# Performance work log

Hardware: AMD Instinct MI355X
Metric: run time of the kernel (lower is better)

The kernel has to match this reference:

```python
import jax, jax.numpy as jnp
import numpy as np

B, H, W, C = 4, 64, 64, 64
C8 = C // 8

def setup_inputs() -> dict:
    key = jax.random.key(0)
    ks = jax.random.split(key, 7)
    x = jax.random.normal(ks[0], (B, H, W, C), dtype=jnp.float32)
    # 1x1 conv weights (channels_first), Glorot-ish scale
    Wf = jax.random.normal(ks[1], (C, C8), dtype=jnp.float32) * (1.0 / np.sqrt(C))
    bf = jnp.zeros((C8,), dtype=jnp.float32)
    Wg = jax.random.normal(ks[2], (C, C8), dtype=jnp.float32) * (1.0 / np.sqrt(C))
    bg = jnp.zeros((C8,), dtype=jnp.float32)
    Wh = jax.random.normal(ks[3], (C, C), dtype=jnp.float32) * (1.0 / np.sqrt(C))
    bh = jnp.zeros((C,), dtype=jnp.float32)
    # original inits gamma=0.0 (output == input); use 0.5 so attention path is exercised
    gamma = jnp.float32(0.5)
    return {"x": x, "Wf": Wf, "bf": bf, "Wg": Wg, "bg": bg, "Wh": Wh, "bh": bh, "gamma": gamma}

def reference(x, Wf, bf, Wg, bg, Wh, bh, gamma):
    Bq, Hq, Wq, Cq = x.shape
    N = Hq * Wq
    # Permute((3,2,1)): (B,H,W,C) -> (B,C,W,H)
    xp = jnp.transpose(x, (0, 3, 2, 1))
    xf = xp.reshape(Bq, Cq, N)  # (B, C, N)
    # 1x1 convs (channels_first) == per-pixel channel matmuls, relu activation
    f = jax.nn.relu(jnp.einsum('ck,bcn->bkn', Wf, xf) + bf[None, :, None])  # (B, C/8, N)
    g = jax.nn.relu(jnp.einsum('ck,bcn->bkn', Wg, xf) + bg[None, :, None])  # (B, C/8, N)
    h = jax.nn.relu(jnp.einsum('cd,bcn->bdn', Wh, xf) + bh[None, :, None])  # (B, C, N)
    # s = g^T f : (B, N, N)
    s = jnp.einsum('bcn,bcm->bnm', g, f)
    b_att = jax.nn.softmax(s, axis=-1)
    # o = h @ b_att : (B, C, N)
    o = jnp.einsum('bck,bkn->bcn', h, b_att)
    y = gamma * o.reshape(xp.shape) + xp
    # Permute((3,2,1)) back: (B,C,W,H) -> (B,H,W,C)
    return jnp.transpose(y, (0, 3, 2, 1))
```

## Files before the change

kernel.cpp:

```cpp
#include <hip/hip_runtime.h>
#include <math.h>

#define B_  4
#define HH  64
#define WW  64
#define CC  64
#define C8_ 8
#define NN  4096
#define BN  (B_*NN)
#define NS  4
#define LOG2E 1.44269504088896340736f

typedef _Float16 half8 __attribute__((ext_vector_type(8)));
typedef float f32x4 __attribute__((ext_vector_type(4)));

#define SWZ(row, kbyte) (((((row) << 7) + (kbyte))) ^ (((row) & 7) << 4))

__global__ __launch_bounds__(256) void prep_kernel(
    const float* __restrict__ x,  const float* __restrict__ Wf, const float* __restrict__ bf,
    const float* __restrict__ Wg, const float* __restrict__ bg, const float* __restrict__ Wh,
    const float* __restrict__ bh, float* __restrict__ f_out, float* __restrict__ g2_out,
    float* __restrict__ h_out)
{
    __shared__ float sWh[CC*CC];
    __shared__ float sWf[CC*C8_];
    __shared__ float sWg[CC*C8_];
    __shared__ float sbf[C8_], sbg[C8_], sbh[CC];
    const int t = threadIdx.x;

    for (int i = t; i < CC*CC/4; i += 256) ((float4*)sWh)[i] = ((const float4*)Wh)[i];
    for (int i = t; i < CC*C8_/4; i += 256) {
        ((float4*)sWf)[i] = ((const float4*)Wf)[i];
        ((float4*)sWg)[i] = ((const float4*)Wg)[i];
    }
    if (t < C8_) { sbf[t] = bf[t]; sbg[t] = bg[t]; }
    if (t < CC)  sbh[t] = bh[t];
    __syncthreads();

    const int p = blockIdx.x * 256 + t;
    const int b = p >> 12;
    const int n = p & (NN - 1);
    const int h = n & 63, w = n >> 6;
    const float4* xr4 = (const float4*)(x + (((size_t)(b*HH + h)*WW + w) * CC));

    float fa[C8_], ga[C8_], ha[CC];
    #pragma unroll
    for (int j = 0; j < C8_; ++j) { fa[j] = sbf[j]; ga[j] = sbg[j]; }
    #pragma unroll
    for (int d = 0; d < CC; ++d) ha[d] = sbh[d];

    #pragma unroll
    for (int c4 = 0; c4 < CC/4; ++c4) {
        float4 v = xr4[c4];
        float xs[4] = {v.x, v.y, v.z, v.w};
        #pragma unroll
        for (int u = 0; u < 4; ++u) {
            const int c = c4*4 + u;
            const float xc = xs[u];
            #pragma unroll
            for (int j = 0; j < C8_; ++j) {
                fa[j] = fmaf(sWf[c*C8_ + j], xc, fa[j]);
                ga[j] = fmaf(sWg[c*C8_ + j], xc, ga[j]);
            }
            #pragma unroll
            for (int d = 0; d < CC; ++d)
                ha[d] = fmaf(sWh[c*CC + d], xc, ha[d]);
        }
    }

    float* fp = f_out  + (size_t)p * C8_;
    float* gp = g2_out + (size_t)p * C8_;
    #pragma unroll
    for (int j4 = 0; j4 < 2; ++j4) {
        float4 fo, go;
        fo.x = fmaxf(fa[j4*4+0], 0.f); fo.y = fmaxf(fa[j4*4+1], 0.f);
        fo.z = fmaxf(fa[j4*4+2], 0.f); fo.w = fmaxf(fa[j4*4+3], 0.f);
        go.x = fmaxf(ga[j4*4+0], 0.f) * LOG2E; go.y = fmaxf(ga[j4*4+1], 0.f) * LOG2E;
        go.z = fmaxf(ga[j4*4+2], 0.f) * LOG2E; go.w = fmaxf(ga[j4*4+3], 0.f) * LOG2E;
        ((float4*)fp)[j4] = fo;
        ((float4*)gp)[j4] = go;
    }
    #pragma unroll
    for (int d = 0; d < CC; ++d)
        h_out[((size_t)(b*CC + d))*NN + n] = fmaxf(ha[d], 0.f);
}

__global__ __launch_bounds__(512) void pass1_kernel(
    const float* __restrict__ f_in, const float* __restrict__ g2_in,
    float* __restrict__ pm_out, float* __restrict__ pz_out)
{
    __shared__ float sF[128*C8_];
    __shared__ float pm[8][64], pz[8][64];
    const int t  = threadIdx.x;
    const int bi = blockIdx.x;
    const int ktile = bi & 63;
    const int b  = (bi >> 6) & 3;
    const int ns = bi >> 8;
    const int k0 = ktile << 6;
    const int kk = t & 63;
    const int q  = t >> 6;
    const int k  = k0 + kk;

    const float4* gp = (const float4*)(g2_in + ((size_t)b*NN + k)*C8_);
    const float4 g0 = gp[0], g1 = gp[1];
    const float4* fb = ((const float4*)f_in) + (size_t)b*8192 + ns*2048;

    float m = 0.f, z = 0.f;
    for (int T = 0; T < 8; ++T) {
        __syncthreads();
        if (t < 256) ((float4*)sF)[t] = fb[T*256 + t];
        __syncthreads();
        const float4* sF4 = (const float4*)sF;
        #pragma unroll 4
        for (int i = 0; i < 16; ++i) {
            const int nl = q*16 + i;
            const float4 f0 = sF4[nl*2], f1 = sF4[nl*2 + 1];
            float s = g0.x*f0.x + g0.y*f0.y + g0.z*f0.z + g0.w*f0.w
                    + g1.x*f1.x + g1.y*f1.y + g1.z*f1.z + g1.w*f1.w;
            if (s > m) { z = z * exp2f(m - s) + 1.f; m = s; }
            else       { z += exp2f(s - m); }
        }
    }
    pm[q][kk] = m; pz[q][kk] = z;
    __syncthreads();
    if (t < 64) {
        float M = pm[0][t];
        #pragma unroll
        for (int qq = 1; qq < 8; ++qq) M = fmaxf(M, pm[qq][t]);
        float Z = 0.f;
        #pragma unroll
        for (int qq = 0; qq < 8; ++qq) Z += pz[qq][t] * exp2f(pm[qq][t] - M);
        pm_out[(size_t)ns*BN + b*NN + k0 + t] = M;
        pz_out[(size_t)ns*BN + b*NN + k0 + t] = Z;
    }
}

__global__ __launch_bounds__(256) void lse_combine_kernel(
    const float* __restrict__ pm, const float* __restrict__ pz,
    float* __restrict__ L2_out)
{
    const int r = blockIdx.x * 256 + threadIdx.x;
    float M = pm[r];
    #pragma unroll
    for (int ns = 1; ns < NS; ++ns) M = fmaxf(M, pm[(size_t)ns*BN + r]);
    float Z = 0.f;
    #pragma unroll
    for (int ns = 0; ns < NS; ++ns)
        Z += pz[(size_t)ns*BN + r] * exp2f(pm[(size_t)ns*BN + r] - M);
    L2_out[r] = M + log2f(Z);
}

#define OFF_SWH 0
#define OFF_SWL 16384
#define OFF_SHH 32768
#define OFF_SHL 40960
#define OFF_SG  49152
#define OFF_SL  51200
#define LDS_SZ  51456

__global__ __launch_bounds__(256, 3) void pass2_kernel(
    const float* __restrict__ f_in, const float* __restrict__ g2_in,
    const float* __restrict__ h_in, const float* __restrict__ L2_in,
    float* __restrict__ opart, int ksplit)
{
    __shared__ __align__(16) unsigned char lds[LDS_SZ];

    const int t     = threadIdx.x;
    const int bi    = blockIdx.x;
    const int nt    = bi & 31;
    const int b     = (bi >> 5) & 3;
    const int chunk = bi >> 7;
    const int n0    = nt << 7;
    const int kchunk = NN / ksplit;
    const int kbase0 = chunk * kchunk;
    const int ktiles = kchunk >> 6;

    const int lane = t & 63, wid = t >> 6;
    const int wn = wid & 1, kh = wid >> 1;
    const int nw = t & 127, kh2 = t >> 7;
    const int sc = t >> 2,  skq = t & 3;

    const float4* fp4 = (const float4*)(f_in + ((size_t)b*NN + n0 + nw)*C8_);
    const float4 fA = fp4[0], fB = fp4[1];

    f32x4 acc[4][4] = {};

    for (int kt = 0; kt < ktiles; ++kt) {
        const int kb = kbase0 + (kt << 6);
        __syncthreads();
        if (t < 128) ((float4*)(lds + OFF_SG))[t] =
            ((const float4*)(g2_in + ((size_t)b*NN + kb)*C8_))[t];
        if (t < 16) ((float4*)(lds + OFF_SL))[t] =
            ((const float4*)(L2_in + (size_t)b*NN + kb))[t];
        {
            const float* hr = h_in + ((size_t)(b*CC + sc))*NN + kb + skq*16;
            float hv[16];
            #pragma unroll
            for (int j = 0; j < 4; ++j) {
                float4 v = ((const float4*)hr)[j];
                hv[j*4+0] = v.x; hv[j*4+1] = v.y; hv[j*4+2] = v.z; hv[j*4+3] = v.w;
            }
            #pragma unroll
            for (int half = 0; half < 2; ++half) {
                union { _Float16 h[8]; uint4 u; } ph, pl;
                #pragma unroll
                for (int j = 0; j < 8; ++j) {
                    float v = hv[half*8 + j];
                    _Float16 hi = (_Float16)v;
                    ph.h[j] = hi;
                    pl.h[j] = (_Float16)(v - (float)hi);
                }
                const int kbyte = (skq*16 + half*8) * 2;
                *(uint4*)(lds + OFF_SHH + SWZ(sc, kbyte)) = ph.u;
                *(uint4*)(lds + OFF_SHL + SWZ(sc, kbyte)) = pl.u;
            }
        }
        __syncthreads();
        {
            const float4* sG4 = (const float4*)(lds + OFF_SG);
            const float*  sLf = (const float*)(lds + OFF_SL);
            #pragma unroll
            for (int kk8 = 0; kk8 < 4; ++kk8) {
                union { _Float16 h[8]; uint4 u; } wh, wl;
                #pragma unroll
                for (int j = 0; j < 8; ++j) {
                    const int kkk = kh2*32 + kk8*8 + j;
                    const float4 q0 = sG4[kkk*2], q1 = sG4[kkk*2+1];
                    float s = q0.x*fA.x + q0.y*fA.y + q0.z*fA.z + q0.w*fA.w
                            + q1.x*fB.x + q1.y*fB.y + q1.z*fB.z + q1.w*fB.w;
                    float wv = exp2f(s - sLf[kkk]);
                    _Float16 hi = (_Float16)wv;
                    wh.h[j] = hi;
                    wl.h[j] = (_Float16)(wv - (float)hi);
                }
                const int kbyte = (kh2*32 + kk8*8) * 2;
                *(uint4*)(lds + OFF_SWH + SWZ(nw, kbyte)) = wh.u;
                *(uint4*)(lds + OFF_SWL + SWZ(nw, kbyte)) = wl.u;
            }
        }
        __syncthreads();
        {
            const int kbyteg = (kh*32 + ((lane >> 4) << 3)) << 1;
            half8 Ah[4], Al[4];
            #pragma unroll
            for (int ai = 0; ai < 4; ++ai) {
                const int n = wn*64 + ai*16 + (lane & 15);
                Ah[ai] = *(const half8*)(lds + OFF_SWH + SWZ(n, kbyteg));
                Al[ai] = *(const half8*)(lds + OFF_SWL + SWZ(n, kbyteg));
            }
            #pragma unroll
            for (int bj = 0; bj < 4; ++bj) {
                const int c = bj*16 + (lane & 15);
                const half8 Bh = *(const half8*)(lds + OFF_SHH + SWZ(c, kbyteg));
                const half8 Bl = *(const half8*)(lds + OFF_SHL + SWZ(c, kbyteg));
                #pragma unroll
                for (int ai = 0; ai < 4; ++ai) {
                    acc[ai][bj] = __builtin_amdgcn_mfma_f32_16x16x32_f16(Ah[ai], Bh, acc[ai][bj], 0, 0, 0);
                    acc[ai][bj] = __builtin_amdgcn_mfma_f32_16x16x32_f16(Ah[ai], Bl, acc[ai][bj], 0, 0, 0);
                    acc[ai][bj] = __builtin_amdgcn_mfma_f32_16x16x32_f16(Al[ai], Bh, acc[ai][bj], 0, 0, 0);
                }
            }
        }
    }

    __syncthreads();
    float* scratch = (float*)lds;
    if (kh == 1) {
        #pragma unroll
        for (int ai = 0; ai < 4; ++ai)
            #pragma unroll
            for (int bj = 0; bj < 4; ++bj)
                #pragma unroll
                for (int r = 0; r < 4; ++r) {
                    const int nloc = ai*16 + (lane >> 4)*4 + r;
                    const int c    = bj*16 + (lane & 15);
                    scratch[wn*4096 + nloc*64 + c] = acc[ai][bj][r];
                }
    }
    __syncthreads();
    if (kh == 0) {
        float* op = opart + (((size_t)chunk*B_ + b)*NN + n0 + wn*64)*CC;
        #pragma unroll
        for (int ai = 0; ai < 4; ++ai)
            #pragma unroll
            for (int bj = 0; bj < 4; ++bj)
                #pragma unroll
                for (int r = 0; r < 4; ++r) {
                    const int nloc = ai*16 + (lane >> 4)*4 + r;
                    const int c    = bj*16 + (lane & 15);
                    op[(size_t)nloc*CC + c] = acc[ai][bj][r] + scratch[wn*4096 + nloc*64 + c];
                }
    }
}

__global__ __launch_bounds__(256) void epi_kernel(
    const float* __restrict__ x, const float* __restrict__ opart,
    const float* __restrict__ gamma_p, float* __restrict__ y, int nchunks)
{
    const int idx = blockIdx.x * 256 + threadIdx.x;
    const float gm = gamma_p[0];
    const int c4 = idx & 15;
    const int n  = (idx >> 4) & (NN - 1);
    const int b  = idx >> 16;
    float4 o; o.x = 0.f; o.y = 0.f; o.z = 0.f; o.w = 0.f;
    for (int ch = 0; ch < nchunks; ++ch) {
        const float4 v = ((const float4*)opart)[((size_t)(ch*B_ + b)*NN + n)*16 + c4];
        o.x += v.x; o.y += v.y; o.z += v.z; o.w += v.w;
    }
    const int h = n & 63, w = n >> 6;
    const size_t xi = ((size_t)((b*HH + h)*WW + w)*CC >> 2) + c4;
    const float4 xv = ((const float4*)x)[xi];
    float4 r;
    r.x = fmaf(gm, o.x, xv.x);
    r.y = fmaf(gm, o.y, xv.y);
    r.z = fmaf(gm, o.z, xv.z);
    r.w = fmaf(gm, o.w, xv.w);
    ((float4*)y)[xi] = r;
}

extern "C" void kernel_launch(void* const* d_in, const int* in_sizes, int n_in,
                              void* d_out, int out_size, void* d_ws, size_t ws_size,
                              hipStream_t stream)
{
    const float* x     = (const float*)d_in[0];
    const float* Wf    = (const float*)d_in[1];
    const float* bf    = (const float*)d_in[2];
    const float* Wg    = (const float*)d_in[3];
    const float* bg    = (const float*)d_in[4];
    const float* Wh    = (const float*)d_in[5];
    const float* bh    = (const float*)d_in[6];
    const float* gamma = (const float*)d_in[7];
    float* out = (float*)d_out;

    float* f_buf  = (float*)d_ws;
    float* g2_buf = f_buf  + (size_t)BN*C8_;
    float* h_buf  = g2_buf + (size_t)BN*C8_;
    float* L2_buf = h_buf  + (size_t)BN*CC;
    float* opart  = L2_buf + (size_t)BN;
    float* pm_buf = opart;
    float* pz_buf = opart + (size_t)NS*BN;

    const size_t fixed = (size_t)(BN*C8_*2 + BN*CC + BN);
    int ksplit = 1;
    if      (ws_size >= (fixed + (size_t)8*BN*CC) * 4) ksplit = 8;
    else if (ws_size >= (fixed + (size_t)4*BN*CC) * 4) ksplit = 4;
    else if (ws_size >= (fixed + (size_t)2*BN*CC) * 4) ksplit = 2;

    prep_kernel<<<BN/256, 256, 0, stream>>>(x, Wf, bf, Wg, bg, Wh, bh,
                                            f_buf, g2_buf, h_buf);
    pass1_kernel<<<NS*B_*64, 512, 0, stream>>>(f_buf, g2_buf, pm_buf, pz_buf);
    lse_combine_kernel<<<BN/256, 256, 0, stream>>>(pm_buf, pz_buf, L2_buf);
    pass2_kernel<<<128*ksplit, 256, 0, stream>>>(f_buf, g2_buf, h_buf, L2_buf,
                                                 opart, ksplit);
    epi_kernel<<<(BN*CC/4)/256, 256, 0, stream>>>(x, opart, gamma, out, ksplit);
}
```

Measured before the change: 207.4 us.

## Use MFMA for score computation, precomputed softmax bound, and restructured prep

The attention scores in pass2 now come from fp16 split-precision MFMA instructions instead of scalar dot products. This needs a per-tile staging of g and f in LDS, and the cross-warp k-split reduction is dropped. Pass1 uses a fixed upper bound (g dot per-batch channel max of f, found by atomicMax in prep) instead of an online running max, which removes branchy rescaling. The prep kernel is restructured to 32 pixels per block with channel groups spread across threads, which cuts register pressure. The maximum k-split drops from 8 to 4. The fixed-bound softmax risks underflow when scores fall far below the bound, and split fp16 scores may lose some accuracy.

New measurement: 180.3 us. 1.15x faster.

```diff
diff --git a/kernel.cpp b/kernel.cpp
--- a/kernel.cpp
+++ b/kernel.cpp
@@ -14,83 +14,121 @@
 typedef _Float16 half8 __attribute__((ext_vector_type(8)));
 typedef float f32x4 __attribute__((ext_vector_type(4)));
 
-#define SWZ(row, kbyte) (((((row) << 7) + (kbyte))) ^ (((row) & 7) << 4))
-
+#define SWZ(row, kbyte) ((((row) << 7) + (kbyte)) ^ (((row) & 7) << 4))
+
+__global__ void zero_fmax_kernel(unsigned* __restrict__ fmax_u) {
+    if (threadIdx.x < B_*C8_) fmax_u[threadIdx.x] = 0u;
+}
+
+#define XSTR 66
 __global__ __launch_bounds__(256) void prep_kernel(
     const float* __restrict__ x,  const float* __restrict__ Wf, const float* __restrict__ bf,
     const float* __restrict__ Wg, const float* __restrict__ bg, const float* __restrict__ Wh,
     const float* __restrict__ bh, float* __restrict__ f_out, float* __restrict__ g2_out,
-    float* __restrict__ h_out)
-{
+    float* __restrict__ h_out, unsigned* __restrict__ fmax_u)
+{
+    __shared__ float sX[32*XSTR];
     __shared__ float sWh[CC*CC];
     __shared__ float sWf[CC*C8_];
     __shared__ float sWg[CC*C8_];
-    __shared__ float sbf[C8_], sbg[C8_], sbh[CC];
-    const int t = threadIdx.x;
+    const int t  = threadIdx.x;
+    const int px = t & 31;
+    const int dg = t >> 5;
 
     for (int i = t; i < CC*CC/4; i += 256) ((float4*)sWh)[i] = ((const float4*)Wh)[i];
-    for (int i = t; i < CC*C8_/4; i += 256) {
-        ((float4*)sWf)[i] = ((const float4*)Wf)[i];
-        ((float4*)sWg)[i] = ((const float4*)Wg)[i];
-    }
-    if (t < C8_) { sbf[t] = bf[t]; sbg[t] = bg[t]; }
-    if (t < CC)  sbh[t] = bh[t];
+    if (t < 128) {
+        ((float4*)sWf)[t] = ((const float4*)Wf)[t];
+        ((float4*)sWg)[t] = ((const float4*)Wg)[t];
+    }
+
+    const int p0 = blockIdx.x * 32;
+    const int b  = p0 >> 12;
+    const int n0 = p0 & (NN - 1);
+    const int h0 = n0 & 63, w = n0 >> 6;
+
+    {
+        const int spx = t >> 3, cq = t & 7;
+        const float* xr = x + (((size_t)(b*HH + h0 + spx)*WW + w) * CC) + cq*8;
+        float4 v0 = ((const float4*)xr)[0], v1 = ((const float4*)xr)[1];
+        float* dst = sX + spx*XSTR + cq*8;
+        dst[0]=v0.x; dst[1]=v0.y; dst[2]=v0.z; dst[3]=v0.w;
+        dst[4]=v1.x; dst[5]=v1.y; dst[6]=v1.z; dst[7]=v1.w;
+    }
     __syncthreads();
 
-    const int p = blockIdx.x * 256 + t;
-    const int b = p >> 12;
-    const int n = p & (NN - 1);
-    const int h = n & 63, w = n >> 6;
-    const float4* xr4 = (const float4*)(x + (((size_t)(b*HH + h)*WW + w) * CC));
-
-    float fa[C8_], ga[C8_], ha[CC];
-    #pragma unroll
-    for (int j = 0; j < C8_; ++j) { fa[j] = sbf[j]; ga[j] = sbg[j]; }
-    #pragma unroll
-    for (int d = 0; d < CC; ++d) ha[d] = sbh[d];
-
-    #pragma unroll
-    for (int c4 = 0; c4 < CC/4; ++c4) {
-        float4 v = xr4[c4];
-        float xs[4] = {v.x, v.y, v.z, v.w};
+    const bool do_fg = dg < 2;
+    const float* sWfg = (dg == 0) ? sWf : sWg;
+    const float* bfg  = (dg == 0) ? bf  : bg;
+
+    float ha[8], fa[8];
+    #pragma unroll
+    for (int j = 0; j < 8; ++j) {
+        ha[j] = bh[dg*8 + j];
+        fa[j] = do_fg ? bfg[j] : 0.f;
+    }
+
+    const float* xrow = sX + px*XSTR;
+    #pragma unroll 4
+    for (int c = 0; c < CC; ++c) {
+        const float xc = xrow[c];
+        const float4 w0 = ((const float4*)sWh)[c*16 + dg*2];
+        const float4 w1 = ((const float4*)sWh)[c*16 + dg*2 + 1];
+        ha[0] = fmaf(w0.x, xc, ha[0]); ha[1] = fmaf(w0.y, xc, ha[1]);
+        ha[2] = fmaf(w0.z, xc, ha[2]); ha[3] = fmaf(w0.w, xc, ha[3]);
+        ha[4] = fmaf(w1.x, xc, ha[4]); ha[5] = fmaf(w1.y, xc, ha[5]);
+        ha[6] = fmaf(w1.z, xc, ha[6]); ha[7] = fmaf(w1.w, xc, ha[7]);
+        if (do_fg) {
+            const float4 f0 = ((const float4*)sWfg)[c*2];
+            const float4 f1 = ((const float4*)sWfg)[c*2 + 1];
+            fa[0] = fmaf(f0.x, xc, fa[0]); fa[1] = fmaf(f0.y, xc, fa[1]);
+            fa[2] = fmaf(f0.z, xc, fa[2]); fa[3] = fmaf(f0.w, xc, fa[3]);
+            fa[4] = fmaf(f1.x, xc, fa[4]); fa[5] = fmaf(f1.y, xc, fa[5]);
+            fa[6] = fmaf(f1.z, xc, fa[6]); fa[7] = fmaf(f1.w, xc, fa[7]);
+        }
+    }
+
+    const int p = p0 + px, n = n0 + px;
+    #pragma unroll
+    for (int j = 0; j < 8; ++j)
+        h_out[((size_t)(b*CC + dg*8 + j))*NN + n] = fmaxf(ha[j], 0.f);
+
+    float fo[8];
+    #pragma unroll
+    for (int j = 0; j < 8; ++j) fo[j] = fmaxf(fa[j], 0.f);
+    if (dg == 0) {
+        float4 a, c4;
+        a.x=fo[0]; a.y=fo[1]; a.z=fo[2]; a.w=fo[3];
+        c4.x=fo[4]; c4.y=fo[5]; c4.z=fo[6]; c4.w=fo[7];
+        ((float4*)(f_out + (size_t)p*C8_))[0] = a;
+        ((float4*)(f_out + (size_t)p*C8_))[1] = c4;
+    } else if (dg == 1) {
+        float4 a, c4;
+        a.x=fo[0]*LOG2E; a.y=fo[1]*LOG2E; a.z=fo[2]*LOG2E; a.w=fo[3]*LOG2E;
+        c4.x=fo[4]*LOG2E; c4.y=fo[5]*LOG2E; c4.z=fo[6]*LOG2E; c4.w=fo[7]*LOG2E;
+        ((float4*)(g2_out + (size_t)p*C8_))[0] = a;
+        ((float4*)(g2_out + (size_t)p*C8_))[1] = c4;
+    }
+
+    __syncthreads();
+    if (dg == 0) {
         #pragma unroll
-        for (int u = 0; u < 4; ++u) {
-            const int c = c4*4 + u;
-            const float xc = xs[u];
-            #pragma unroll
-            for (int j = 0; j < C8_; ++j) {
-                fa[j] = fmaf(sWf[c*C8_ + j], xc, fa[j]);
-                ga[j] = fmaf(sWg[c*C8_ + j], xc, ga[j]);
-            }
-            #pragma unroll
-            for (int d = 0; d < CC; ++d)
-                ha[d] = fmaf(sWh[c*CC + d], xc, ha[d]);
-        }
-    }
-
-    float* fp = f_out  + (size_t)p * C8_;
-    float* gp = g2_out + (size_t)p * C8_;
-    #pragma unroll
-    for (int j4 = 0; j4 < 2; ++j4) {
-        float4 fo, go;
-        fo.x = fmaxf(fa[j4*4+0], 0.f); fo.y = fmaxf(fa[j4*4+1], 0.f);
-        fo.z = fmaxf(fa[j4*4+2], 0.f); fo.w = fmaxf(fa[j4*4+3], 0.f);
-        go.x = fmaxf(ga[j4*4+0], 0.f) * LOG2E; go.y = fmaxf(ga[j4*4+1], 0.f) * LOG2E;
-        go.z = fmaxf(ga[j4*4+2], 0.f) * LOG2E; go.w = fmaxf(ga[j4*4+3], 0.f) * LOG2E;
-        ((float4*)fp)[j4] = fo;
-        ((float4*)gp)[j4] = go;
-    }
-    #pragma unroll
-    for (int d = 0; d < CC; ++d)
-        h_out[((size_t)(b*CC + d))*NN + n] = fmaxf(ha[d], 0.f);
+        for (int j = 0; j < 8; ++j) sX[px*8 + j] = fo[j];
+    }
+    __syncthreads();
+    if (t < 8) {
+        float mx = sX[t];
+        for (int q = 1; q < 32; ++q) mx = fmaxf(mx, sX[q*8 + t]);
+        atomicMax(&fmax_u[b*C8_ + t], __float_as_uint(mx));
+    }
 }
 
 __global__ __launch_bounds__(512) void pass1_kernel(
     const float* __restrict__ f_in, const float* __restrict__ g2_in,
-    float* __restrict__ pm_out, float* __restrict__ pz_out)
+    const float* __restrict__ fmax_f, float* __restrict__ pz_out,
+    float* __restrict__ bound_out)
 {
     __shared__ float sF[128*C8_];
-    __shared__ float pm[8][64], pz[8][64];
+    __shared__ float pzs[8][64];
     const int t  = threadIdx.x;
     const int bi = blockIdx.x;
     const int ktile = bi & 63;
@@ -103,67 +141,65 @@
 
     const float4* gp = (const float4*)(g2_in + ((size_t)b*NN + k)*C8_);
     const float4 g0 = gp[0], g1 = gp[1];
+    const float4* fm4 = (const float4*)(fmax_f + b*C8_);
+    const float4 m0 = fm4[0], m1 = fm4[1];
+    const float bound = g0.x*m0.x + g0.y*m0.y + g0.z*m0.z + g0.w*m0.w
+                      + g1.x*m1.x + g1.y*m1.y + g1.z*m1.z + g1.w*m1.w;
+
     const float4* fb = ((const float4*)f_in) + (size_t)b*8192 + ns*2048;
 
-    float m = 0.f, z = 0.f;
+    float z = 0.f;
     for (int T = 0; T < 8; ++T) {
         __syncthreads();
         if (t < 256) ((float4*)sF)[t] = fb[T*256 + t];
         __syncthreads();
         const float4* sF4 = (const float4*)sF;
-        #pragma unroll 4
+        #pragma unroll 8
         for (int i = 0; i < 16; ++i) {
             const int nl = q*16 + i;
             const float4 f0 = sF4[nl*2], f1 = sF4[nl*2 + 1];
             float s = g0.x*f0.x + g0.y*f0.y + g0.z*f0.z + g0.w*f0.w
                     + g1.x*f1.x + g1.y*f1.y + g1.z*f1.z + g1.w*f1.w;
-            if (s > m) { z = z * exp2f(m - s) + 1.f; m = s; }
-            else       { z += exp2f(s - m); }
-        }
-    }
-    pm[q][kk] = m; pz[q][kk] = z;
+            z += exp2f(s - bound);
+        }
+    }
+    pzs[q][kk] = z;
     __syncthreads();
     if (t < 64) {
-        float M = pm[0][t];
+        float Z = pzs[0][t];
         #pragma unroll
-        for (int qq = 1; qq < 8; ++qq) M = fmaxf(M, pm[qq][t]);
-        float Z = 0.f;
-        #pragma unroll
-        for (int qq = 0; qq < 8; ++qq) Z += pz[qq][t] * exp2f(pm[qq][t] - M);
-        pm_out[(size_t)ns*BN + b*NN + k0 + t] = M;
+        for (int qq = 1; qq < 8; ++qq) Z += pzs[qq][t];
         pz_out[(size_t)ns*BN + b*NN + k0 + t] = Z;
+        if (ns == 0) bound_out[(size_t)b*NN + k0 + t] = bound;
     }
 }
 
 __global__ __launch_bounds__(256) void lse_combine_kernel(
-    const float* __restrict__ pm, const float* __restrict__ pz,
+    const float* __restrict__ pz, const float* __restrict__ bound_in,
     float* __restrict__ L2_out)
 {
     const int r = blockIdx.x * 256 + threadIdx.x;
-    float M = pm[r];
-    #pragma unroll
-    for (int ns = 1; ns < NS; ++ns) M = fmaxf(M, pm[(size_t)ns*BN + r]);
     float Z = 0.f;
     #pragma unroll
-    for (int ns = 0; ns < NS; ++ns)
-        Z += pz[(size_t)ns*BN + r] * exp2f(pm[(size_t)ns*BN + r] - M);
-    L2_out[r] = M + log2f(Z);
-}
-
-#define OFF_SWH 0
-#define OFF_SWL 16384
-#define OFF_SHH 32768
-#define OFF_SHL 40960
-#define OFF_SG  49152
-#define OFF_SL  51200
-#define LDS_SZ  51456
-
-__global__ __launch_bounds__(256, 3) void pass2_kernel(
+    for (int ns = 0; ns < NS; ++ns) Z += pz[(size_t)ns*BN + r];
+    L2_out[r] = bound_in[r] + log2f(fmaxf(Z, 1e-37f));
+}
+
+#define P2_SWH 0
+#define P2_SWL 16384
+#define P2_SHH 32768
+#define P2_SHL 40960
+#define P2_SFP 49152
+#define P2_SGP 59392
+#define P2_SL  64512
+#define P2_LDS 64768
+
+__global__ __launch_bounds__(256, 2) void pass2_kernel(
     const float* __restrict__ f_in, const float* __restrict__ g2_in,
     const float* __restrict__ h_in, const float* __restrict__ L2_in,
     float* __restrict__ opart, int ksplit)
 {
-    __shared__ __align__(16) unsigned char lds[LDS_SZ];
+    __shared__ __align__(16) unsigned char lds[P2_LDS];
 
     const int t     = threadIdx.x;
     const int bi    = blockIdx.x;
@@ -176,121 +212,136 @@
     const int ktiles = kchunk >> 6;
 
     const int lane = t & 63, wid = t >> 6;
-    const int wn = wid & 1, kh = wid >> 1;
-    const int nw = t & 127, kh2 = t >> 7;
-    const int sc = t >> 2,  skq = t & 3;
-
-    const float4* fp4 = (const float4*)(f_in + ((size_t)b*NN + n0 + nw)*C8_);
-    const float4 fA = fp4[0], fB = fp4[1];
-
-    f32x4 acc[4][4] = {};
+    const int lg = lane >> 4, l15 = lane & 15;
+    const uint4 zq = {0u, 0u, 0u, 0u};
+
+    if (t < 128) {
+        const float4* fp4 = (const float4*)(f_in + ((size_t)b*NN + n0 + t)*C8_);
+        const float4 a = fp4[0], c4 = fp4[1];
+        float v[8] = {a.x,a.y,a.z,a.w,c4.x,c4.y,c4.z,c4.w};
+        union { _Float16 h[8]; uint4 u; } qh, ql;
+        #pragma unroll
+        for (int j = 0; j < 8; ++j) {
+            _Float16 hi = (_Float16)v[j];
+            qh.h[j] = hi; ql.h[j] = (_Float16)(v[j] - (float)hi);
+        }
+        unsigned char* base = lds + P2_SFP + t*80;
+        *(uint4*)(base)      = qh.u;
+        *(uint4*)(base + 16) = ql.u;
+        *(uint4*)(base + 32) = qh.u;
+        *(uint4*)(base + 48) = zq;
+    }
+    __syncthreads();
+
+    half8 fB[8];
+    #pragma unroll
+    for (int ntl = 0; ntl < 8; ++ntl)
+        fB[ntl] = *(const half8*)(lds + P2_SFP + (ntl*16 + l15)*80 + lg*16);
+
+    f32x4 oacc[2][4] = {};
 
     for (int kt = 0; kt < ktiles; ++kt) {
         const int kb = kbase0 + (kt << 6);
         __syncthreads();
-        if (t < 128) ((float4*)(lds + OFF_SG))[t] =
-            ((const float4*)(g2_in + ((size_t)b*NN + kb)*C8_))[t];
-        if (t < 16) ((float4*)(lds + OFF_SL))[t] =
+        if (t < 128) {
+            const int k = t >> 1, hf = t & 1;
+            const float4* gp4 = (const float4*)(g2_in + ((size_t)b*NN + kb + k)*C8_);
+            const float4 a = gp4[0], c4 = gp4[1];
+            float v[8] = {a.x,a.y,a.z,a.w,c4.x,c4.y,c4.z,c4.w};
+            union { _Float16 h[8]; uint4 u; } qh, ql;
+            #pragma unroll
+            for (int j = 0; j < 8; ++j) {
+                _Float16 hi = (_Float16)v[j];
+                qh.h[j] = hi; ql.h[j] = (_Float16)(v[j] - (float)hi);
+            }
+            unsigned char* base = lds + P2_SGP + k*80;
+            if (hf == 0) { *(uint4*)(base) = qh.u; *(uint4*)(base + 16) = qh.u; }
+            else         { *(uint4*)(base + 32) = ql.u; *(uint4*)(base + 48) = zq; }
+        }
+        if (t < 16) ((float4*)(lds + P2_SL))[t] =
             ((const float4*)(L2_in + (size_t)b*NN + kb))[t];
         {
-            const float* hr = h_in + ((size_t)(b*CC + sc))*NN + kb + skq*16;
-            float hv[16];
+            const int c = t >> 2, kq4 = t & 3;
+            const float4* hp4 = (const float4*)(h_in + ((size_t)(b*CC + c))*NN + kb + kq4*16);
+            float v[16];
             #pragma unroll
             for (int j = 0; j < 4; ++j) {
-                float4 v = ((const float4*)hr)[j];
-                hv[j*4+0] = v.x; hv[j*4+1] = v.y; hv[j*4+2] = v.z; hv[j*4+3] = v.w;
-            }
-            #pragma unroll
-            for (int half = 0; half < 2; ++half) {
-                union { _Float16 h[8]; uint4 u; } ph, pl;
+                float4 w4 = hp4[j];
+                v[j*4+0]=w4.x; v[j*4+1]=w4.y; v[j*4+2]=w4.z; v[j*4+3]=w4.w;
+            }
+            #pragma unroll
+            for (int hseg = 0; hseg < 2; ++hseg) {
+                union { _Float16 h[8]; uint4 u; } qh, ql;
                 #pragma unroll
                 for (int j = 0; j < 8; ++j) {
-                    float v = hv[half*8 + j];
-                    _Float16 hi = (_Float16)v;
-                    ph.h[j] = hi;
-                    pl.h[j] = (_Float16)(v - (float)hi);
+                    float vv = v[hseg*8 + j];
+                    _Float16 hi = (_Float16)vv;
+                    qh.h[j] = hi; ql.h[j] = (_Float16)(vv - (float)hi);
                 }
-                const int kbyte = (skq*16 + half*8) * 2;
-                *(uint4*)(lds + OFF_SHH + SWZ(sc, kbyte)) = ph.u;
-                *(uint4*)(lds + OFF_SHL + SWZ(sc, kbyte)) = pl.u;
+                const int kbyte = kq4*32 + hseg*16;
+                *(uint4*)(lds + P2_SHH + SWZ(c, kbyte)) = qh.u;
+                *(uint4*)(lds + P2_SHL + SWZ(c, kbyte)) = ql.u;
             }
         }
         __syncthreads();
+
         {
-            const float4* sG4 = (const float4*)(lds + OFF_SG);
-            const float*  sLf = (const float*)(lds + OFF_SL);
-            #pragma unroll
-            for (int kk8 = 0; kk8 < 4; ++kk8) {
-                union { _Float16 h[8]; uint4 u; } wh, wl;
-                #pragma unroll
-                for (int j = 0; j < 8; ++j) {
-                    const int kkk = kh2*32 + kk8*8 + j;
-                    const float4 q0 = sG4[kkk*2], q1 = sG4[kkk*2+1];
-                    float s = q0.x*fA.x + q0.y*fA.y + q0.z*fA.z + q0.w*fA.w
-                            + q1.x*fB.x + q1.y*fB.y + q1.z*fB.z + q1.w*fB.w;
-                    float wv = exp2f(s - sLf[kkk]);
-                    _Float16 hi = (_Float16)wv;
-                    wh.h[j] = hi;
-                    wl.h[j] = (_Float16)(wv - (float)hi);
-                }
-                const int kbyte = (kh2*32 + kk8*8) * 2;
-                *(uint4*)(lds + OFF_SWH + SWZ(nw, kbyte)) = wh.u;
-                *(uint4*)(lds + OFF_SWL + SWZ(nw, kbyte)) = wl.u;
-            }
-        }
-        __syncthreads();
-        {
-            const int kbyteg = (kh*32 + ((lane >> 4) << 3)) << 1;
-            half8 Ah[4], Al[4];
-            #pragma unroll
-            for (int ai = 0; ai < 4; ++ai) {
-                const int n = wn*64 + ai*16 + (lane & 15);
-                Ah[ai] = *(const half8*)(lds + OFF_SWH + SWZ(n, kbyteg));
-                Al[ai] = *(const half8*)(lds + OFF_SWL + SWZ(n, kbyteg));
-            }
-            #pragma unroll
-            for (int bj = 0; bj < 4; ++bj) {
-                const int c = bj*16 + (lane & 15);
-                const half8 Bh = *(const half8*)(lds + OFF_SHH + SWZ(c, kbyteg));
-                const half8 Bl = *(const half8*)(lds + OFF_SHL + SWZ(c, kbyteg));
-                #pragma unroll
-                for (int ai = 0; ai < 4; ++ai) {
-                    acc[ai][bj] = __builtin_amdgcn_mfma_f32_16x16x32_f16(Ah[ai], Bh, acc[ai][bj], 0, 0, 0);
-                    acc[ai][bj] = __builtin_amdgcn_mfma_f32_16x16x32_f16(Ah[ai], Bl, acc[ai][bj], 0, 0, 0);
-                    acc[ai][bj] = __builtin_amdgcn_mfma_f32_16x16x32_f16(Al[ai], Bh, acc[ai][bj], 0, 0, 0);
-                }
-            }
-        }
-    }
-
-    __syncthreads();
-    float* scratch = (float*)lds;
-    if (kh == 1) {
-        #pragma unroll
-        for (int ai = 0; ai < 4; ++ai)
-            #pragma unroll
-            for (int bj = 0; bj < 4; ++bj)
+            const half8 Ag = *(const half8*)(lds + P2_SGP + (wid*16 + l15)*80 + lg*16);
+            const float4 L2v = *(const float4*)(lds + P2_SL + wid*64 + lg*16);
+            f32x4 sacc[8] = {};
+            #pragma unroll
+            for (int ntl = 0; ntl < 8; ++ntl)
+                sacc[ntl] = __builtin_amdgcn_mfma_f32_16x16x32_f16(Ag, fB[ntl], sacc[ntl], 0, 0, 0);
+            #pragma unroll
+            for (int ntl = 0; ntl < 8; ++ntl) {
+                union { _Float16 h[4]; uint2 u; } wh, wl;
                 #pragma unroll
                 for (int r = 0; r < 4; ++r) {
-                    const int nloc = ai*16 + (lane >> 4)*4 + r;
-                    const int c    = bj*16 + (lane & 15);
-                    scratch[wn*4096 + nloc*64 + c] = acc[ai][bj][r];
+                    float wv = exp2f(sacc[ntl][r] - L2v[r]);
+                    _Float16 hi = (_Float16)wv;
+                    wh.h[r] = hi; wl.h[r] = (_Float16)(wv - (float)hi);
                 }
-    }
-    __syncthreads();
-    if (kh == 0) {
-        float* op = opart + (((size_t)chunk*B_ + b)*NN + n0 + wn*64)*CC;
+                const int n = ntl*16 + l15;
+                const int kbyte = wid*32 + lg*8;
+                *(uint2*)(lds + P2_SWH + SWZ(n, kbyte)) = wh.u;
+                *(uint2*)(lds + P2_SWL + SWZ(n, kbyte)) = wl.u;
+            }
+        }
+        __syncthreads();
+
         #pragma unroll
-        for (int ai = 0; ai < 4; ++ai)
-            #pragma unroll
-            for (int bj = 0; bj < 4; ++bj)
+        for (int ks = 0; ks < 2; ++ks) {
+            const int kbyteg = ks*64 + lg*16;
+            half8 Ah[2], Al[2];
+            #pragma unroll
+            for (int at = 0; at < 2; ++at) {
+                const int n = wid*32 + at*16 + l15;
+                Ah[at] = *(const half8*)(lds + P2_SWH + SWZ(n, kbyteg));
+                Al[at] = *(const half8*)(lds + P2_SWL + SWZ(n, kbyteg));
+            }
+            #pragma unroll
+            for (int ct = 0; ct < 4; ++ct) {
+                const int c = ct*16 + l15;
+                const half8 Bh = *(const half8*)(lds + P2_SHH + SWZ(c, kbyteg));
+                const half8 Bl = *(const half8*)(lds + P2_SHL + SWZ(c, kbyteg));
                 #pragma unroll
-                for (int r = 0; r < 4; ++r) {
-                    const int nloc = ai*16 + (lane >> 4)*4 + r;
-                    const int c    = bj*16 + (lane & 15);
-                    op[(size_t)nloc*CC + c] = acc[ai][bj][r] + scratch[wn*4096 + nloc*64 + c];
+                for (int at = 0; at < 2; ++at) {
+                    oacc[at][ct] = __builtin_amdgcn_mfma_f32_16x16x32_f16(Ah[at], Bh, oacc[at][ct], 0, 0, 0);
+                    oacc[at][ct] = __builtin_amdgcn_mfma_f32_16x16x32_f16(Ah[at], Bl, oacc[at][ct], 0, 0, 0);
+                    oacc[at][ct] = __builtin_amdgcn_mfma_f32_16x16x32_f16(Al[at], Bh, oacc[at][ct], 0, 0, 0);
                 }
-    }
+            }
+        }
+    }
+
+    float* op = opart + (((size_t)chunk*B_ + b)*NN + n0 + wid*32)*CC;
+    #pragma unroll
+    for (int at = 0; at < 2; ++at)
+        #pragma unroll
+        for (int ct = 0; ct < 4; ++ct)
+            #pragma unroll
+            for (int r = 0; r < 4; ++r)
+                op[(size_t)(at*16 + lg*4 + r)*CC + ct*16 + l15] = oacc[at][ct][r];
 }
 
 __global__ __launch_bounds__(256) void epi_kernel(
@@ -332,24 +383,25 @@
     const float* gamma = (const float*)d_in[7];
     float* out = (float*)d_out;
 
-    float* f_buf  = (float*)d_ws;
-    float* g2_buf = f_buf  + (size_t)BN*C8_;
-    float* h_buf  = g2_buf + (size_t)BN*C8_;
-    float* L2_buf = h_buf  + (size_t)BN*CC;
-    float* opart  = L2_buf + (size_t)BN;
-    float* pm_buf = opart;
-    float* pz_buf = opart + (size_t)NS*BN;
-
-    const size_t fixed = (size_t)(BN*C8_*2 + BN*CC + BN);
+    float* f_buf   = (float*)d_ws;
+    float* g2_buf  = f_buf    + (size_t)BN*C8_;
+    float* h_buf   = g2_buf   + (size_t)BN*C8_;
+    float* L2_buf  = h_buf    + (size_t)BN*CC;
+    float* pz_buf  = L2_buf   + (size_t)BN;
+    float* bnd_buf = pz_buf   + (size_t)NS*BN;
+    float* fmax_b  = bnd_buf  + (size_t)BN;
+    float* opart   = fmax_b   + 32;
+
+    const size_t fixedf = (size_t)BN*(C8_*2 + CC + 1 + NS + 1) + 32;
     int ksplit = 1;
-    if      (ws_size >= (fixed + (size_t)8*BN*CC) * 4) ksplit = 8;
-    else if (ws_size >= (fixed + (size_t)4*BN*CC) * 4) ksplit = 4;
-    else if (ws_size >= (fixed + (size_t)2*BN*CC) * 4) ksplit = 2;
-
-    prep_kernel<<<BN/256, 256, 0, stream>>>(x, Wf, bf, Wg, bg, Wh, bh,
-                                            f_buf, g2_buf, h_buf);
-    pass1_kernel<<<NS*B_*64, 512, 0, stream>>>(f_buf, g2_buf, pm_buf, pz_buf);
-    lse_combine_kernel<<<BN/256, 256, 0, stream>>>(pm_buf, pz_buf, L2_buf);
+    if      (ws_size >= (fixedf + (size_t)4*BN*CC) * 4) ksplit = 4;
+    else if (ws_size >= (fixedf + (size_t)2*BN*CC) * 4) ksplit = 2;
+
+    zero_fmax_kernel<<<1, 64, 0, stream>>>((unsigned*)fmax_b);
+    prep_kernel<<<BN/32, 256, 0, stream>>>(x, Wf, bf, Wg, bg, Wh, bh,
+                                           f_buf, g2_buf, h_buf, (unsigned*)fmax_b);
+    pass1_kernel<<<NS*B_*64, 512, 0, stream>>>(f_buf, g2_buf, fmax_b, pz_buf, bnd_buf);
+    lse_combine_kernel<<<BN/256, 256, 0, stream>>>(pz_buf, bnd_buf, L2_buf);
     pass2_kernel<<<128*ksplit, 256, 0, stream>>>(f_buf, g2_buf, h_buf, L2_buf,
                                                  opart, ksplit);
     epi_kernel<<<(BN*CC/4)/256, 256, 0, stream>>>(x, opart, gamma, out, ksplit);
```
